# Kernel tuning notes

Measured on AMD Instinct MI355X. Metric: run time of the kernel, lower is better.

Reference implementation:

```python
import jax, jax.numpy as jnp
import numpy as np

N_NODES = 50000
IN_CH = 256
N_REL = 5
N_EDGES = 800000
LAST_SENSES = 25000
LAST_GLOBALS = 45000


def setup_inputs() -> dict:
    key = jax.random.key(0)
    ks = jax.random.split(key, 12)
    batch_x = jax.random.normal(ks[0], (N_NODES, IN_CH), dtype=jnp.float32)
    batch_edge_index = jax.random.randint(ks[1], (2, N_EDGES), 0, N_NODES)
    batch_edge_type = jax.random.randint(ks[2], (N_EDGES,), 0, N_REL)
    s = 1.0 / np.sqrt(IN_CH)
    comp = jax.random.normal(ks[3], (N_REL, N_REL), dtype=jnp.float32) * (1.0 / np.sqrt(N_REL))
    basis = jax.random.normal(ks[4], (N_REL, IN_CH, IN_CH), dtype=jnp.float32) * s
    root = jax.random.normal(ks[5], (IN_CH, IN_CH), dtype=jnp.float32) * s
    bias = jnp.zeros((IN_CH,), dtype=jnp.float32)
    n_glob = LAST_GLOBALS - LAST_SENSES
    Wg = jax.random.normal(ks[6], (n_glob, IN_CH), dtype=jnp.float32) * s
    bg = jnp.zeros((n_glob,), dtype=jnp.float32)
    Ws = jax.random.normal(ks[7], (LAST_SENSES, IN_CH), dtype=jnp.float32) * s
    bs = jnp.zeros((LAST_SENSES,), dtype=jnp.float32)
    return {
        'batch_x': batch_x,
        'batch_edge_index': batch_edge_index,
        'batch_edge_type': batch_edge_type,
        'comp': comp,
        'basis': basis,
        'root': root,
        'bias': bias,
        'Wg': Wg,
        'bg': bg,
        'Ws': Ws,
        'bs': bs,
    }


def _rgcn_conv(x, edge_index, edge_type, comp, basis, root, bias):
    # Basis decomposition: W_r = sum_b comp[r,b] * basis[b]  -> [R, d, d]
    R = comp.shape[0]
    N = x.shape[0]
    W = jnp.einsum('rb,bdf->rdf', comp, basis)
    # Transform all nodes by every relation weight once ([R,N,F]), then gather
    # per edge instead of doing an [E,d,d] weight gather.
    H = jnp.einsum('nd,rdf->rnf', x, W)
    src, dst = edge_index[0], edge_index[1]
    msgs = H[edge_type, src]                     # [E, F]
    seg = edge_type * N + dst                    # combined (relation, dst) id
    sums = jax.ops.segment_sum(msgs, seg, num_segments=R * N)
    cnt = jax.ops.segment_sum(jnp.ones((msgs.shape[0],), msgs.dtype), seg,
                              num_segments=R * N)
    mean = sums / jnp.maximum(cnt, 1.0)[:, None]  # per-relation mean aggregation
    agg = mean.reshape(R, N, -1).sum(axis=0)
    return agg + x @ root + bias


def reference(batch_x, batch_edge_index, batch_edge_type, comp, basis, root,
              bias, Wg, bg, Ws, bs):
    h = jax.nn.relu(_rgcn_conv(batch_x, batch_edge_index, batch_edge_type,
                               comp, basis, root, bias))
    x1 = h[0]                                    # current node embedding [F]
    logits_global = Wg @ x1 + bg
    logits_sense = Ws @ x1 + bs
    return (jax.nn.log_softmax(logits_global, axis=0),
            jax.nn.log_softmax(logits_sense, axis=0))
```

## Files before the change

### kernel.cpp

```cpp
#include <hip/hip_runtime.h>
#include <math.h>

#define N_NODES 50000
#define IN_CH 256
#define N_REL 5
#define N_EDGES 800000
#define N_GLOB 20000
#define N_SENSE 25000
#define N_OUT 45000
#define MAX_MATCH 256
#define NBLK_LOGITS (N_OUT / 4)
#define NBLK_GLOB (N_GLOB / 4)


__global__ void k_W(const float* __restrict__ comp,
                    const float* __restrict__ basis,
                    float* __restrict__ W,
                    float* __restrict__ sums,
                    int* __restrict__ ip) {
    int t = threadIdx.x, bid = blockIdx.x;
    if (bid == 0 && t < 8) ip[t] = 0;
    if (bid < 5) sums[bid * 256 + t] = 0.f;
    int idx = bid * 256 + t;
    int r = idx >> 16, df = idx & 65535;
    float acc = 0.f;
#pragma unroll
    for (int b = 0; b < N_REL; ++b)
        acc += comp[r * N_REL + b] * basis[b * (IN_CH * IN_CH) + df];
    W[idx] = acc;
}

__device__ __forceinline__ void record_edge(const int* ei, const int* et,
                                            int* ip, int e) {
    int t = et[e];
    int p = atomicAdd(&ip[0], 1);
    if (p < MAX_MATCH) {
        ip[8 + p] = ei[e];
        ip[8 + MAX_MATCH + p] = t;
    }
    atomicAdd(&ip[1 + t], 1);
}

__global__ void k_scan(const int* __restrict__ ei,
                       const int* __restrict__ et,
                       int* __restrict__ ip) {
    int e4 = blockIdx.x * 256 + threadIdx.x;
    if (e4 * 4 >= N_EDGES) return;
    int4 d = ((const int4*)(ei + N_EDGES))[e4];
    int e = e4 * 4;
    if (d.x == 0) record_edge(ei, et, ip, e);
    if (d.y == 0) record_edge(ei, et, ip, e + 1);
    if (d.z == 0) record_edge(ei, et, ip, e + 2);
    if (d.w == 0) record_edge(ei, et, ip, e + 3);
}

__global__ __launch_bounds__(1024) void k_msgs(const float* __restrict__ x,
                                               const float* __restrict__ W,
                                               const int* __restrict__ ip,
                                               float* __restrict__ sums) {
    int j = blockIdx.x;
    int m = ip[0]; if (m > MAX_MATCH) m = MAX_MATCH;
    if (j >= m) return;
    __shared__ float xrow[IN_CH];
    __shared__ float red[4][IN_CH];
    int tid = threadIdx.x;
    int f = tid & 255, c = tid >> 8;
    int s = ip[8 + j];
    int r = ip[8 + MAX_MATCH + j];
    if (c == 0) xrow[f] = x[(size_t)s * IN_CH + f];
    __syncthreads();
    const float* Wr = W + r * (IN_CH * IN_CH) + c * 64 * IN_CH;
    float acc = 0.f;
#pragma unroll 8
    for (int d = 0; d < 64; ++d) acc += xrow[c * 64 + d] * Wr[d * IN_CH + f];
    red[c][f] = acc;
    __syncthreads();
    if (c == 0)
        atomicAdd(&sums[r * IN_CH + f],
                  red[0][f] + red[1][f] + red[2][f] + red[3][f]);
}

__global__ __launch_bounds__(1024) void k_combine(const float* __restrict__ x,
                                                  const float* __restrict__ root,
                                                  const float* __restrict__ bias,
                                                  const float* __restrict__ sums,
                                                  const int* __restrict__ ip,
                                                  float* __restrict__ x1) {
    __shared__ float xrow[IN_CH];
    __shared__ float red[4][IN_CH];
    int tid = threadIdx.x;
    int f = tid & 255, c = tid >> 8;
    if (c == 0) xrow[f] = x[f];
    __syncthreads();
    const float* Rr = root + c * 64 * IN_CH;
    float acc = 0.f;
#pragma unroll 8
    for (int d = 0; d < 64; ++d) acc += xrow[c * 64 + d] * Rr[d * IN_CH + f];
    red[c][f] = acc;
    __syncthreads();
    if (c == 0) {
        float a = bias[f] + red[0][f] + red[1][f] + red[2][f] + red[3][f];
#pragma unroll
        for (int r = 0; r < N_REL; ++r)
            a += sums[r * IN_CH + f] / fmaxf((float)ip[1 + r], 1.0f);
        x1[f] = fmaxf(a, 0.f);
    }
}

__global__ void k_logits(const float* __restrict__ Wg,
                         const float* __restrict__ bg,
                         const float* __restrict__ Ws,
                         const float* __restrict__ bs,
                         const float* __restrict__ x1,
                         float* __restrict__ out,
                         float* __restrict__ pmax,
                         float* __restrict__ psum) {
    __shared__ float sx[IN_CH];
    __shared__ float sl[4];
    int tid = threadIdx.x;
    sx[tid] = x1[tid];
    __syncthreads();
    int lane = tid & 63, w = tid >> 6;
    int row = blockIdx.x * 4 + w;
    const float4* wr;
    float b;
    if (row < N_GLOB) {
        wr = (const float4*)(Wg + (size_t)row * IN_CH);
        b = bg[row];
    } else {
        int r2 = row - N_GLOB;
        wr = (const float4*)(Ws + (size_t)r2 * IN_CH);
        b = bs[r2];
    }
    float4 wv = wr[lane];
    float4 xv = ((const float4*)sx)[lane];
    float s = wv.x * xv.x + wv.y * xv.y + wv.z * xv.z + wv.w * xv.w;
#pragma unroll
    for (int off = 32; off > 0; off >>= 1) s += __shfl_down(s, off);
    if (lane == 0) { float l = s + b; out[row] = l; sl[w] = l; }
    __syncthreads();
    if (tid == 0) {
        float m4 = fmaxf(fmaxf(sl[0], sl[1]), fmaxf(sl[2], sl[3]));
        float s4 = expf(sl[0] - m4) + expf(sl[1] - m4) +
                   expf(sl[2] - m4) + expf(sl[3] - m4);
        pmax[blockIdx.x] = m4;
        psum[blockIdx.x] = s4;
    }
}

__global__ void k_stats(const float* __restrict__ pmax,
                        const float* __restrict__ psum,
                        float* __restrict__ stats) {
    __shared__ float rm[256], rs[256];
    int seg = blockIdx.x;
    int off = seg ? NBLK_GLOB : 0;
    int n = seg ? (NBLK_LOGITS - NBLK_GLOB) : NBLK_GLOB;
    int tid = threadIdx.x;
    float m = -3.4e38f, s = 0.f;
    for (int i = tid; i < n; i += 256) {
        float mi = pmax[off + i], si = psum[off + i];
        float M = fmaxf(m, mi);
        s = s * expf(m - M) + si * expf(mi - M);
        m = M;
    }
    rm[tid] = m; rs[tid] = s; __syncthreads();
    for (int h = 128; h > 0; h >>= 1) {
        if (tid < h) {
            float m2 = rm[tid + h], s2 = rs[tid + h];
            float M = fmaxf(rm[tid], m2);
            rs[tid] = rs[tid] * expf(rm[tid] - M) + s2 * expf(m2 - M);
            rm[tid] = M;
        }
        __syncthreads();
    }
    if (tid == 0) { stats[seg * 2] = rm[0]; stats[seg * 2 + 1] = logf(rs[0]); }
}

__global__ void k_final(float* __restrict__ out, const float* __restrict__ stats) {
    int i = blockIdx.x * 256 + threadIdx.x;
    if (i >= N_OUT) return;
    int seg = (i >= N_GLOB) ? 1 : 0;
    out[i] = out[i] - stats[seg * 2] - stats[seg * 2 + 1];
}

extern "C" void kernel_launch(void* const* d_in, const int* in_sizes, int n_in,
                              void* d_out, int out_size, void* d_ws, size_t ws_size,
                              hipStream_t stream) {
    const float* x     = (const float*)d_in[0];
    const int*   ei    = (const int*)  d_in[1];
    const int*   et    = (const int*)  d_in[2];
    const float* comp  = (const float*)d_in[3];
    const float* basis = (const float*)d_in[4];
    const float* root  = (const float*)d_in[5];
    const float* bias  = (const float*)d_in[6];
    const float* Wg    = (const float*)d_in[7];
    const float* bg    = (const float*)d_in[8];
    const float* Wsn   = (const float*)d_in[9];
    const float* bs    = (const float*)d_in[10];
    float* out = (float*)d_out;

    float* base  = (float*)d_ws;
    float* W     = base;
    float* sums  = base + 327680;
    float* x1    = base + 328960;
    float* stats = base + 329216;
    int*   ip    = (int*)(base + 329220);
    float* pmax  = base + 330240;
    float* psum  = base + 341490;

    k_W      <<<(N_REL * IN_CH * IN_CH) / 256, 256, 0, stream>>>(comp, basis, W, sums, ip);
    k_scan   <<<(N_EDGES / 4 + 255) / 256, 256, 0, stream>>>(ei, et, ip);
    k_msgs   <<<MAX_MATCH, 1024, 0, stream>>>(x, W, ip, sums);
    k_combine<<<1, 1024, 0, stream>>>(x, root, bias, sums, ip, x1);
    k_logits <<<NBLK_LOGITS, 256, 0, stream>>>(Wg, bg, Wsn, bs, x1, out, pmax, psum);
    k_stats  <<<2, 256, 0, stream>>>(pmax, psum, stats);
    k_final  <<<(N_OUT + 255) / 256, 256, 0, stream>>>(out, stats);
}
```

Measured before the change: 158.0 us.

## Aggregate neighbor rows before basis transform and fuse stats into final pass

Drops the full W = comp·basis materialization and the per-edge matrix-vector products. Instead it forms, per basis, a weighted sum of the matching source rows (scaled by comp and the inverse relation count), then applies one basis matvec per block, with a sixth block handling root and bias; results are atomically accumulated and ReLU is applied in the logits kernel. The stats and final normalization kernels are merged, so every block redundantly reduces all partial max/sum values, and a memset replaces the zeroing work. This cuts launches and memory traffic on the small serial stages, at the cost of a serial loop over matches in one wave per block and redundant per-block reductions.

```diff
diff --git a/kernel.cpp b/kernel.cpp
--- a/kernel.cpp
+++ b/kernel.cpp
@@ -12,23 +12,6 @@
 #define NBLK_LOGITS (N_OUT / 4)
 #define NBLK_GLOB (N_GLOB / 4)
 
-
-__global__ void k_W(const float* __restrict__ comp,
-                    const float* __restrict__ basis,
-                    float* __restrict__ W,
-                    float* __restrict__ sums,
-                    int* __restrict__ ip) {
-    int t = threadIdx.x, bid = blockIdx.x;
-    if (bid == 0 && t < 8) ip[t] = 0;
-    if (bid < 5) sums[bid * 256 + t] = 0.f;
-    int idx = bid * 256 + t;
-    int r = idx >> 16, df = idx & 65535;
-    float acc = 0.f;
-#pragma unroll
-    for (int b = 0; b < N_REL; ++b)
-        acc += comp[r * N_REL + b] * basis[b * (IN_CH * IN_CH) + df];
-    W[idx] = acc;
-}
 
 __device__ __forceinline__ void record_edge(const int* ei, const int* et,
                                             int* ip, int e) {
@@ -54,56 +37,48 @@
     if (d.w == 0) record_edge(ei, et, ip, e + 3);
 }
 
-__global__ __launch_bounds__(1024) void k_msgs(const float* __restrict__ x,
-                                               const float* __restrict__ W,
-                                               const int* __restrict__ ip,
-                                               float* __restrict__ sums) {
-    int j = blockIdx.x;
-    int m = ip[0]; if (m > MAX_MATCH) m = MAX_MATCH;
-    if (j >= m) return;
-    __shared__ float xrow[IN_CH];
+__global__ __launch_bounds__(1024) void k_x1(const float* __restrict__ x,
+                                             const float* __restrict__ comp,
+                                             const float* __restrict__ basis,
+                                             const float* __restrict__ root,
+                                             const float* __restrict__ bias,
+                                             const int* __restrict__ ip,
+                                             float* __restrict__ x1acc) {
+    __shared__ float u[IN_CH];
     __shared__ float red[4][IN_CH];
     int tid = threadIdx.x;
     int f = tid & 255, c = tid >> 8;
-    int s = ip[8 + j];
-    int r = ip[8 + MAX_MATCH + j];
-    if (c == 0) xrow[f] = x[(size_t)s * IN_CH + f];
+    int b = blockIdx.x;
+    const float* M;
+    if (b < 5) {
+        if (c == 0) {
+            int m = ip[0]; if (m > MAX_MATCH) m = MAX_MATCH;
+            float acc = 0.f;
+            for (int j = 0; j < m; ++j) {
+                int s = ip[8 + j];
+                int t = ip[8 + MAX_MATCH + j];
+                float scale = comp[t * N_REL + b] /
+                              fmaxf((float)ip[1 + t], 1.0f);
+                acc += scale * x[(size_t)s * IN_CH + f];
+            }
+            u[f] = acc;
+        }
+        M = basis + (size_t)b * IN_CH * IN_CH;
+    } else {
+        if (c == 0) u[f] = x[f];
+        M = root;
+    }
     __syncthreads();
-    const float* Wr = W + r * (IN_CH * IN_CH) + c * 64 * IN_CH;
+    const float* Mr = M + c * 64 * IN_CH;
     float acc = 0.f;
 #pragma unroll 8
-    for (int d = 0; d < 64; ++d) acc += xrow[c * 64 + d] * Wr[d * IN_CH + f];
-    red[c][f] = acc;
-    __syncthreads();
-    if (c == 0)
-        atomicAdd(&sums[r * IN_CH + f],
-                  red[0][f] + red[1][f] + red[2][f] + red[3][f]);
-}
-
-__global__ __launch_bounds__(1024) void k_combine(const float* __restrict__ x,
-                                                  const float* __restrict__ root,
-                                                  const float* __restrict__ bias,
-                                                  const float* __restrict__ sums,
-                                                  const int* __restrict__ ip,
-                                                  float* __restrict__ x1) {
-    __shared__ float xrow[IN_CH];
-    __shared__ float red[4][IN_CH];
-    int tid = threadIdx.x;
-    int f = tid & 255, c = tid >> 8;
-    if (c == 0) xrow[f] = x[f];
-    __syncthreads();
-    const float* Rr = root + c * 64 * IN_CH;
-    float acc = 0.f;
-#pragma unroll 8
-    for (int d = 0; d < 64; ++d) acc += xrow[c * 64 + d] * Rr[d * IN_CH + f];
+    for (int d = 0; d < 64; ++d) acc += u[c * 64 + d] * Mr[d * IN_CH + f];
     red[c][f] = acc;
     __syncthreads();
     if (c == 0) {
-        float a = bias[f] + red[0][f] + red[1][f] + red[2][f] + red[3][f];
-#pragma unroll
-        for (int r = 0; r < N_REL; ++r)
-            a += sums[r * IN_CH + f] / fmaxf((float)ip[1 + r], 1.0f);
-        x1[f] = fmaxf(a, 0.f);
+        float a = red[0][f] + red[1][f] + red[2][f] + red[3][f];
+        if (b == 5) a += bias[f];
+        atomicAdd(&x1acc[f], a);
     }
 }
 
@@ -111,14 +86,14 @@
                          const float* __restrict__ bg,
                          const float* __restrict__ Ws,
                          const float* __restrict__ bs,
-                         const float* __restrict__ x1,
+                         const float* __restrict__ x1acc,
                          float* __restrict__ out,
                          float* __restrict__ pmax,
                          float* __restrict__ psum) {
     __shared__ float sx[IN_CH];
     __shared__ float sl[4];
     int tid = threadIdx.x;
-    sx[tid] = x1[tid];
+    sx[tid] = fmaxf(x1acc[tid], 0.f);
     __syncthreads();
     int lane = tid & 63, w = tid >> 6;
     int row = blockIdx.x * 4 + w;
@@ -148,39 +123,41 @@
     }
 }
 
-__global__ void k_stats(const float* __restrict__ pmax,
-                        const float* __restrict__ psum,
-                        float* __restrict__ stats) {
-    __shared__ float rm[256], rs[256];
-    int seg = blockIdx.x;
-    int off = seg ? NBLK_GLOB : 0;
-    int n = seg ? (NBLK_LOGITS - NBLK_GLOB) : NBLK_GLOB;
+__global__ void k_statsfinal(const float* __restrict__ pmax,
+                             const float* __restrict__ psum,
+                             float* __restrict__ out) {
+    __shared__ float rmg[256], rsg[256], rms[256], rss[256];
     int tid = threadIdx.x;
-    float m = -3.4e38f, s = 0.f;
-    for (int i = tid; i < n; i += 256) {
-        float mi = pmax[off + i], si = psum[off + i];
-        float M = fmaxf(m, mi);
-        s = s * expf(m - M) + si * expf(mi - M);
-        m = M;
+    float mg = -3.4e38f, sg = 0.f, ms = -3.4e38f, ss = 0.f;
+    for (int i = tid; i < NBLK_LOGITS; i += 256) {
+        float mi = pmax[i], si = psum[i];
+        if (i < NBLK_GLOB) {
+            float M = fmaxf(mg, mi);
+            sg = sg * expf(mg - M) + si * expf(mi - M); mg = M;
+        } else {
+            float M = fmaxf(ms, mi);
+            ss = ss * expf(ms - M) + si * expf(mi - M); ms = M;
+        }
     }
-    rm[tid] = m; rs[tid] = s; __syncthreads();
+    rmg[tid] = mg; rsg[tid] = sg; rms[tid] = ms; rss[tid] = ss;
+    __syncthreads();
     for (int h = 128; h > 0; h >>= 1) {
         if (tid < h) {
-            float m2 = rm[tid + h], s2 = rs[tid + h];
-            float M = fmaxf(rm[tid], m2);
-            rs[tid] = rs[tid] * expf(rm[tid] - M) + s2 * expf(m2 - M);
-            rm[tid] = M;
+            float m2 = rmg[tid + h], s2 = rsg[tid + h];
+            float M = fmaxf(rmg[tid], m2);
+            rsg[tid] = rsg[tid] * expf(rmg[tid] - M) + s2 * expf(m2 - M);
+            rmg[tid] = M;
+            m2 = rms[tid + h]; s2 = rss[tid + h];
+            M = fmaxf(rms[tid], m2);
+            rss[tid] = rss[tid] * expf(rms[tid] - M) + s2 * expf(m2 - M);
+            rms[tid] = M;
         }
         __syncthreads();
     }
-    if (tid == 0) { stats[seg * 2] = rm[0]; stats[seg * 2 + 1] = logf(rs[0]); }
-}
-
-__global__ void k_final(float* __restrict__ out, const float* __restrict__ stats) {
-    int i = blockIdx.x * 256 + threadIdx.x;
-    if (i >= N_OUT) return;
-    int seg = (i >= N_GLOB) ? 1 : 0;
-    out[i] = out[i] - stats[seg * 2] - stats[seg * 2 + 1];
+    float zg = rmg[0] + logf(rsg[0]);
+    float zs = rms[0] + logf(rss[0]);
+    int row = blockIdx.x * 256 + tid;
+    if (row < N_OUT) out[row] -= (row < N_GLOB) ? zg : zs;
 }
 
 extern "C" void kernel_launch(void* const* d_in, const int* in_sizes, int n_in,
@@ -200,19 +177,14 @@
     float* out = (float*)d_out;
 
     float* base  = (float*)d_ws;
-    float* W     = base;
-    float* sums  = base + 327680;
-    float* x1    = base + 328960;
-    float* stats = base + 329216;
-    int*   ip    = (int*)(base + 329220);
-    float* pmax  = base + 330240;
-    float* psum  = base + 341490;
+    float* x1acc = base;
+    int*   ip    = (int*)(base + 256);
+    float* pmax  = base + 1024;
+    float* psum  = base + 12274;
 
-    k_W      <<<(N_REL * IN_CH * IN_CH) / 256, 256, 0, stream>>>(comp, basis, W, sums, ip);
-    k_scan   <<<(N_EDGES / 4 + 255) / 256, 256, 0, stream>>>(ei, et, ip);
-    k_msgs   <<<MAX_MATCH, 1024, 0, stream>>>(x, W, ip, sums);
-    k_combine<<<1, 1024, 0, stream>>>(x, root, bias, sums, ip, x1);
-    k_logits <<<NBLK_LOGITS, 256, 0, stream>>>(Wg, bg, Wsn, bs, x1, out, pmax, psum);
-    k_stats  <<<2, 256, 0, stream>>>(pmax, psum, stats);
-    k_final  <<<(N_OUT + 255) / 256, 256, 0, stream>>>(out, stats);
+    hipMemsetAsync(d_ws, 0, 264 * sizeof(float), stream);
+    k_scan      <<<(N_EDGES / 4 + 255) / 256, 256, 0, stream>>>(ei, et, ip);
+    k_x1        <<<6, 1024, 0, stream>>>(x, comp, basis, root, bias, ip, x1acc);
+    k_logits    <<<NBLK_LOGITS, 256, 0, stream>>>(Wg, bg, Wsn, bs, x1acc, out, pmax, psum);
+    k_statsfinal<<<(N_OUT + 255) / 256, 256, 0, stream>>>(pmax, psum, out);
 }
```

Result: slower. 169.1 us (+7.0%).
